# Performance work log

Hardware: AMD Instinct MI355X
Metric: run time of the kernel (lower is better)

## Reference

```python
import jax, jax.numpy as jnp
import numpy as np

N = 2048
IN_C, HID, LAT = 128, 128, 64
E_SPARSE = 65536


def gcn_conv(x, W, b, src, dst, w, n):
    # PyG GCNConv: h = D^-1/2 (A+I) D^-1/2 (x W) + b  (self-loops already in edge list)
    deg = jax.ops.segment_sum(w, dst, num_segments=n)
    dinv = jnp.where(deg > 0, jax.lax.rsqrt(deg), 0.0)
    norm = dinv[src] * w * dinv[dst]            # [E]
    h = x @ W                                   # [N, out]
    agg = jax.ops.segment_sum(h[src] * norm[:, None], dst, num_segments=n)
    return agg + b


def setup_inputs() -> dict:
    key = jax.random.key(0)
    ks = jax.random.split(key, 9)
    x = jax.random.normal(ks[0], (N, IN_C), jnp.float32)
    masked_y = jax.random.normal(ks[1], (N, N), jnp.float32)
    edge_index = jax.random.randint(ks[2], (2, E_SPARSE), 0, N, dtype=jnp.int32)
    s = 0.05
    W1 = jax.random.normal(ks[3], (IN_C, HID), jnp.float32) * s
    b1 = jnp.zeros((HID,), jnp.float32)
    Wmu = jax.random.normal(ks[4], (HID, LAT), jnp.float32) * s
    bmu = jnp.zeros((LAT,), jnp.float32)
    Wls = jax.random.normal(ks[5], (HID, LAT), jnp.float32) * s
    bls = jnp.zeros((LAT,), jnp.float32)
    return {"x": x, "masked_y": masked_y, "W1": W1, "b1": b1,
            "Wmu": Wmu, "bmu": bmu, "Wls": Wls, "bls": bls,
            "edge_index": edge_index}


def reference(x, masked_y, W1, b1, Wmu, bmu, Wls, bls, edge_index):
    n = x.shape[0]
    half = n // 2
    # masking leaves only the top-left [half, half] block of masked_y nonzero;
    # dense_to_sparse on that block -> all half*half (row, col) pairs (entries != 0 a.s.)
    rows = jnp.repeat(jnp.arange(half, dtype=edge_index.dtype), half)
    cols = jnp.tile(jnp.arange(half, dtype=edge_index.dtype), half)
    y_w = jax.nn.sigmoid(masked_y[:half, :half].reshape(-1))
    loop = jnp.arange(n, dtype=edge_index.dtype)
    src = jnp.concatenate([edge_index[0], rows, loop])
    dst = jnp.concatenate([edge_index[1], cols, loop])
    w = jnp.concatenate([jnp.ones((edge_index.shape[1],), x.dtype), y_w,
                         jnp.ones((n,), x.dtype)])
    hidden = jax.nn.relu(gcn_conv(x, W1, b1, src, dst, w, n))
    z_mu = gcn_conv(hidden, Wmu, bmu, src, dst, w, n)
    z_logstd = gcn_conv(hidden, Wls, bls, src, dst, w, n)
    return (z_mu, z_logstd)
```

## Files before the change

### kernel.cpp

```cpp
#include <hip/hip_runtime.h>

#define NN 2048
#define HALF 1024
#define CC 128
#define EE 65536
#define CAP 128

typedef unsigned short u16;

__device__ __forceinline__ float sigm(float v){ return 1.0f/(1.0f + __expf(-v)); }

__device__ __forceinline__ float dinv_lo(int i, const int* __restrict__ cnt,
                                         const float* __restrict__ colsum){
  return rsqrtf(1.0f + (float)cnt[i] + colsum[i]);
}
__device__ __forceinline__ float dinv_any(int i, const int* __restrict__ cnt,
                                          const float* __restrict__ colsum){
  float cs = (i < HALF) ? colsum[i] : 0.0f;
  return rsqrtf(1.0f + (float)cnt[i] + cs);
}

__global__ __launch_bounds__(256) void k_prep(
    const float* __restrict__ my, const int* __restrict__ ei,
    const float* __restrict__ bmu, const float* __restrict__ bls,
    float* __restrict__ SpRaw, float* __restrict__ colsum,
    int* __restrict__ cnt, u16* __restrict__ bucket,
    float* __restrict__ out)
{
  int b = blockIdx.x, t = threadIdx.x;
  if (b < 128) {
    int c0 = t*4;
    float cs0=0.f, cs1=0.f, cs2=0.f, cs3=0.f;
    #pragma unroll 2
    for (int rr=0; rr<8; ++rr){
      int r = b*8 + rr;
      float4 v = *(const float4*)(my + (size_t)r*NN + c0);
      float s0=sigm(v.x), s1=sigm(v.y), s2=sigm(v.z), s3=sigm(v.w);
      *(float4*)(SpRaw + (size_t)r*HALF + c0) = make_float4(s0,s1,s2,s3);
      cs0+=s0; cs1+=s1; cs2+=s2; cs3+=s3;
    }
    atomicAdd(&colsum[c0+0], cs0);
    atomicAdd(&colsum[c0+1], cs1);
    atomicAdd(&colsum[c0+2], cs2);
    atomicAdd(&colsum[c0+3], cs3);
  } else {
    int bb = b - 128;
    int gid = bb*256 + t;
    int g4 = (gid & 15)*4;
    const float* bbias = (gid < 32768) ? bmu : bls;
    ((float4*)out)[gid] = make_float4(bbias[g4], bbias[g4+1], bbias[g4+2], bbias[g4+3]);
    int e = bb*256 + t;
    int s = ei[e], d = ei[EE + e];
    int slot = atomicAdd(&cnt[d], 1);
    if (slot < CAP) bucket[d*CAP + slot] = (u16)s;
  }
}

__global__ __launch_bounds__(256) void k_agg1(
  const float* __restrict__ SpRaw, const float* __restrict__ x,
  const int* __restrict__ cnt, const float* __restrict__ colsum,
  const u16* __restrict__ bucket,
  float* __restrict__ SP, float* __restrict__ DP)
{
  int b = blockIdx.x, t = threadIdx.x;
  if (b < 512) {
    __shared__ float srow[128];
    int chunk = b & 7, r0 = chunk*128;
    if (t < 128) srow[t] = dinv_lo(r0 + t, cnt, colsum);
    __syncthreads();
    int lane = t & 63, f0 = lane*2;
    int dbase = (b>>3)*16 + (t>>6)*4;
    float a00=0.f,a01=0.f,a10=0.f,a11=0.f,a20=0.f,a21=0.f,a30=0.f,a31=0.f;
    #pragma unroll 2
    for (int rr=0; rr<128; rr+=4){
      int r = r0 + rr;
      float2 v0 = *(const float2*)(x + (size_t)(r+0)*CC + f0);
      float2 v1 = *(const float2*)(x + (size_t)(r+1)*CC + f0);
      float2 v2 = *(const float2*)(x + (size_t)(r+2)*CC + f0);
      float2 v3 = *(const float2*)(x + (size_t)(r+3)*CC + f0);
      float4 s0 = *(const float4*)(SpRaw + (size_t)(r+0)*HALF + dbase);
      float4 s1 = *(const float4*)(SpRaw + (size_t)(r+1)*HALF + dbase);
      float4 s2 = *(const float4*)(SpRaw + (size_t)(r+2)*HALF + dbase);
      float4 s3 = *(const float4*)(SpRaw + (size_t)(r+3)*HALF + dbase);
      float c0 = srow[rr+0], c1 = srow[rr+1], c2 = srow[rr+2], c3 = srow[rr+3];
      float fx, fy;
      fx = v0.x*c0; fy = v0.y*c0;
      a00=fmaf(s0.x,fx,a00); a01=fmaf(s0.x,fy,a01);
      a10=fmaf(s0.y,fx,a10); a11=fmaf(s0.y,fy,a11);
      a20=fmaf(s0.z,fx,a20); a21=fmaf(s0.z,fy,a21);
      a30=fmaf(s0.w,fx,a30); a31=fmaf(s0.w,fy,a31);
      fx = v1.x*c1; fy = v1.y*c1;
      a00=fmaf(s1.x,fx,a00); a01=fmaf(s1.x,fy,a01);
      a10=fmaf(s1.y,fx,a10); a11=fmaf(s1.y,fy,a11);
      a20=fmaf(s1.z,fx,a20); a21=fmaf(s1.z,fy,a21);
      a30=fmaf(s1.w,fx,a30); a31=fmaf(s1.w,fy,a31);
      fx = v2.x*c2; fy = v2.y*c2;
      a00=fmaf(s2.x,fx,a00); a01=fmaf(s2.x,fy,a01);
      a10=fmaf(s2.y,fx,a10); a11=fmaf(s2.y,fy,a11);
      a20=fmaf(s2.z,fx,a20); a21=fmaf(s2.z,fy,a21);
      a30=fmaf(s2.w,fx,a30); a31=fmaf(s2.w,fy,a31);
      fx = v3.x*c3; fy = v3.y*c3;
      a00=fmaf(s3.x,fx,a00); a01=fmaf(s3.x,fy,a01);
      a10=fmaf(s3.y,fx,a10); a11=fmaf(s3.y,fy,a11);
      a20=fmaf(s3.z,fx,a20); a21=fmaf(s3.z,fy,a21);
      a30=fmaf(s3.w,fx,a30); a31=fmaf(s3.w,fy,a31);
    }
    float d0=dinv_lo(dbase+0,cnt,colsum), d1=dinv_lo(dbase+1,cnt,colsum);
    float d2=dinv_lo(dbase+2,cnt,colsum), d3=dinv_lo(dbase+3,cnt,colsum);
    float* o = DP + ((size_t)chunk*HALF + dbase)*CC + f0;
    o[0*CC+0]=a00*d0; o[0*CC+1]=a01*d0;
    o[1*CC+0]=a10*d1; o[1*CC+1]=a11*d1;
    o[2*CC+0]=a20*d2; o[2*CC+1]=a21*d2;
    o[3*CC+0]=a30*d3; o[3*CC+1]=a31*d3;
  } else {
    __shared__ float sdinv[NN];
    #pragma unroll
    for (int i=0;i<8;i++){
      int j = i*256 + t;
      float cs = (j < HALF) ? colsum[j] : 0.0f;
      sdinv[j] = rsqrtf(1.0f + (float)cnt[j] + cs);
    }
    __syncthreads();
    int w = t>>6, hw = (t>>5)&1, l = t&31;
    int d = (b-512)*8 + w*2 + hw;
    int f0 = l*4;
    float dd = sdinv[d];
    float4 sv = *(const float4*)(x + (size_t)d*CC + f0);
    float ax=dd*sv.x, ay=dd*sv.y, az=dd*sv.z, aw=dd*sv.w;
    int m = cnt[d]; m = m > CAP ? CAP : m;
    const u16* bk = bucket + d*CAP;
    int j = 0;
    for (; j+1 < m; j += 2){
      unsigned pr = *(const unsigned*)(bk + j);
      int s0 = pr & 0xffff, s1 = pr >> 16;
      float w0 = sdinv[s0], w1 = sdinv[s1];
      float4 v0 = *(const float4*)(x + (size_t)s0*CC + f0);
      float4 v1 = *(const float4*)(x + (size_t)s1*CC + f0);
      ax=fmaf(w0,v0.x,ax); ay=fmaf(w0,v0.y,ay); az=fmaf(w0,v0.z,az); aw=fmaf(w0,v0.w,aw);
      ax=fmaf(w1,v1.x,ax); ay=fmaf(w1,v1.y,ay); az=fmaf(w1,v1.z,az); aw=fmaf(w1,v1.w,aw);
    }
    if (j < m){
      int s0 = bk[j];
      float w0 = sdinv[s0];
      float4 v0 = *(const float4*)(x + (size_t)s0*CC + f0);
      ax=fmaf(w0,v0.x,ax); ay=fmaf(w0,v0.y,ay); az=fmaf(w0,v0.z,az); aw=fmaf(w0,v0.w,aw);
    }
    *(float4*)(SP + (size_t)d*CC + f0) = make_float4(dd*ax, dd*ay, dd*az, dd*aw);
  }
}

__global__ __launch_bounds__(256) void k_mid(
  const float* __restrict__ SP, const float* __restrict__ DP,
  const float* __restrict__ b1, const float* __restrict__ W1,
  const float* __restrict__ Wmu, const float* __restrict__ Wls,
  const int* __restrict__ cnt, const float* __restrict__ colsum,
  float* __restrict__ Gm)
{
  __shared__ float la[4][CC];
  __shared__ float lb[4][CC];
  int b = blockIdx.x, t = threadIdx.x;
  int row0 = b*4;
  #pragma unroll
  for (int i=0;i<2;i++){
    int idx = i*256 + t;
    int r = row0 + (idx>>7), c = idx & 127;
    float v = SP[(size_t)r*CC + c];
    if (r < HALF){
      #pragma unroll
      for (int k=0;k<8;k++) v += DP[((size_t)k*HALF + r)*CC + c];
    }
    la[idx>>7][c] = v;
  }
  __syncthreads();
  int f = t & 127, rh = t >> 7;
  {
    const float4* a0 = (const float4*)la[rh*2+0];
    const float4* a1 = (const float4*)la[rh*2+1];
    float o0=0.f, o1=0.f;
    #pragma unroll 4
    for (int k4=0;k4<32;k4++){
      float4 v0=a0[k4], v1=a1[k4];
      float w0 = W1[(k4*4+0)*CC + f];
      float w1 = W1[(k4*4+1)*CC + f];
      float w2 = W1[(k4*4+2)*CC + f];
      float w3 = W1[(k4*4+3)*CC + f];
      o0=fmaf(v0.x,w0,o0); o0=fmaf(v0.y,w1,o0); o0=fmaf(v0.z,w2,o0); o0=fmaf(v0.w,w3,o0);
      o1=fmaf(v1.x,w0,o1); o1=fmaf(v1.y,w1,o1); o1=fmaf(v1.z,w2,o1); o1=fmaf(v1.w,w3,o1);
    }
    float bb = b1[f];
    o0 += bb; o1 += bb;
    lb[rh*2+0][f] = o0 > 0.f ? o0 : 0.f;
    lb[rh*2+1][f] = o1 > 0.f ? o1 : 0.f;
  }
  __syncthreads();
  {
    int g = f & 63;
    const float* W = (f < 64) ? Wmu : Wls;
    const float4* a0 = (const float4*)lb[rh*2+0];
    const float4* a1 = (const float4*)lb[rh*2+1];
    float o0=0.f, o1=0.f;
    #pragma unroll 4
    for (int k4=0;k4<32;k4++){
      float4 v0=a0[k4], v1=a1[k4];
      float w0 = W[(k4*4+0)*64 + g];
      float w1 = W[(k4*4+1)*64 + g];
      float w2 = W[(k4*4+2)*64 + g];
      float w3 = W[(k4*4+3)*64 + g];
      o0=fmaf(v0.x,w0,o0); o0=fmaf(v0.y,w1,o0); o0=fmaf(v0.z,w2,o0); o0=fmaf(v0.w,w3,o0);
      o1=fmaf(v1.x,w0,o1); o1=fmaf(v1.y,w1,o1); o1=fmaf(v1.z,w2,o1); o1=fmaf(v1.w,w3,o1);
    }
    int rA = row0 + rh*2;
    Gm[(size_t)(rA+0)*CC + f] = o0 * dinv_any(rA+0, cnt, colsum);
    Gm[(size_t)(rA+1)*CC + f] = o1 * dinv_any(rA+1, cnt, colsum);
  }
}

__global__ __launch_bounds__(256) void k_agg2(
  const float* __restrict__ SpRaw, const float* __restrict__ Gm,
  const int* __restrict__ cnt, const float* __restrict__ colsum,
  const u16* __restrict__ bucket, float* __restrict__ out)
{
  int b = blockIdx.x, t = threadIdx.x;
  if (b < 512) {
    int lane = t & 63, f0 = lane*2;
    size_t obase = (f0 < 64) ? 0 : (size_t)NN*64;
    int g0 = f0 & 63;
    int dbase = (b>>3)*16 + (t>>6)*4;
    int r0 = (b&7)*128;
    float a00=0.f,a01=0.f,a10=0.f,a11=0.f,a20=0.f,a21=0.f,a30=0.f,a31=0.f;
    #pragma unroll 2
    for (int rr=0; rr<128; rr+=4){
      int r = r0 + rr;
      float2 v0 = *(const float2*)(Gm + (size_t)(r+0)*CC + f0);
      float2 v1 = *(const float2*)(Gm + (size_t)(r+1)*CC + f0);
      float2 v2 = *(const float2*)(Gm + (size_t)(r+2)*CC + f0);
      float2 v3 = *(const float2*)(Gm + (size_t)(r+3)*CC + f0);
      float4 s0 = *(const float4*)(SpRaw + (size_t)(r+0)*HALF + dbase);
      float4 s1 = *(const float4*)(SpRaw + (size_t)(r+1)*HALF + dbase);
      float4 s2 = *(const float4*)(SpRaw + (size_t)(r+2)*HALF + dbase);
      float4 s3 = *(const float4*)(SpRaw + (size_t)(r+3)*HALF + dbase);
      a00=fmaf(s0.x,v0.x,a00); a01=fmaf(s0.x,v0.y,a01);
      a10=fmaf(s0.y,v0.x,a10); a11=fmaf(s0.y,v0.y,a11);
      a20=fmaf(s0.z,v0.x,a20); a21=fmaf(s0.z,v0.y,a21);
      a30=fmaf(s0.w,v0.x,a30); a31=fmaf(s0.w,v0.y,a31);
      a00=fmaf(s1.x,v1.x,a00); a01=fmaf(s1.x,v1.y,a01);
      a10=fmaf(s1.y,v1.x,a10); a11=fmaf(s1.y,v1.y,a11);
      a20=fmaf(s1.z,v1.x,a20); a21=fmaf(s1.z,v1.y,a21);
      a30=fmaf(s1.w,v1.x,a30); a31=fmaf(s1.w,v1.y,a31);
      a00=fmaf(s2.x,v2.x,a00); a01=fmaf(s2.x,v2.y,a01);
      a10=fmaf(s2.y,v2.x,a10); a11=fmaf(s2.y,v2.y,a11);
      a20=fmaf(s2.z,v2.x,a20); a21=fmaf(s2.z,v2.y,a21);
      a30=fmaf(s2.w,v2.x,a30); a31=fmaf(s2.w,v2.y,a31);
      a00=fmaf(s3.x,v3.x,a00); a01=fmaf(s3.x,v3.y,a01);
      a10=fmaf(s3.y,v3.x,a10); a11=fmaf(s3.y,v3.y,a11);
      a20=fmaf(s3.z,v3.x,a20); a21=fmaf(s3.z,v3.y,a21);
      a30=fmaf(s3.w,v3.x,a30); a31=fmaf(s3.w,v3.y,a31);
    }
    float d0=dinv_lo(dbase+0,cnt,colsum), d1=dinv_lo(dbase+1,cnt,colsum);
    float d2=dinv_lo(dbase+2,cnt,colsum), d3=dinv_lo(dbase+3,cnt,colsum);
    float* o = out + obase + (size_t)dbase*64 + g0;
    atomicAdd(o + 0*64 + 0, a00*d0); atomicAdd(o + 0*64 + 1, a01*d0);
    atomicAdd(o + 1*64 + 0, a10*d1); atomicAdd(o + 1*64 + 1, a11*d1);
    atomicAdd(o + 2*64 + 0, a20*d2); atomicAdd(o + 2*64 + 1, a21*d2);
    atomicAdd(o + 3*64 + 0, a30*d3); atomicAdd(o + 3*64 + 1, a31*d3);
  } else {
    int w = t>>6, hw = (t>>5)&1, l = t&31;
    int d = (b-512)*8 + w*2 + hw;
    int f0 = l*4;
    size_t obase = (f0 < 64) ? 0 : (size_t)NN*64;
    int g0 = f0 & 63;
    float4 a = *(const float4*)(Gm + (size_t)d*CC + f0);
    float ax=a.x, ay=a.y, az=a.z, aw=a.w;
    int m = cnt[d]; m = m > CAP ? CAP : m;
    const u16* bk = bucket + d*CAP;
    int j = 0;
    for (; j+1 < m; j += 2){
      unsigned pr = *(const unsigned*)(bk + j);
      int s0 = pr & 0xffff, s1 = pr >> 16;
      float4 v0 = *(const float4*)(Gm + (size_t)s0*CC + f0);
      float4 v1 = *(const float4*)(Gm + (size_t)s1*CC + f0);
      ax += v0.x + v1.x; ay += v0.y + v1.y;
      az += v0.z + v1.z; aw += v0.w + v1.w;
    }
    if (j < m){
      int s0 = bk[j];
      float4 v0 = *(const float4*)(Gm + (size_t)s0*CC + f0);
      ax += v0.x; ay += v0.y; az += v0.z; aw += v0.w;
    }
    float dd = dinv_any(d, cnt, colsum);
    float* o = out + obase + (size_t)d*64 + g0;
    atomicAdd(o + 0, dd*ax); atomicAdd(o + 1, dd*ay);
    atomicAdd(o + 2, dd*az); atomicAdd(o + 3, dd*aw);
  }
}

extern "C" void kernel_launch(void* const* d_in, const int* in_sizes, int n_in,
                              void* d_out, int out_size, void* d_ws, size_t ws_size,
                              hipStream_t stream)
{
  (void)in_sizes; (void)n_in; (void)out_size; (void)ws_size;
  const float* x   = (const float*)d_in[0];
  const float* my  = (const float*)d_in[1];
  const float* W1  = (const float*)d_in[2];
  const float* b1  = (const float*)d_in[3];
  const float* Wmu = (const float*)d_in[4];
  const float* bmu = (const float*)d_in[5];
  const float* Wls = (const float*)d_in[6];
  const float* bls = (const float*)d_in[7];
  const int*   ei  = (const int*)d_in[8];
  float* out = (float*)d_out;
  char* ws = (char*)d_ws;

  int*   cnt    = (int*)  (ws + 0);
  float* colsum = (float*)(ws + 8192);
  u16*   bucket = (u16*)  (ws + 12288);
  float* SpRaw  = (float*)(ws + 536576);
  float* Gm     = (float*)(ws + 4730880);
  float* SP     = (float*)(ws + 5779456);
  float* DP     = (float*)(ws + 6828032);

  hipMemsetAsync(ws, 0, 12288, stream);
  k_prep<<<384, 256, 0, stream>>>(my, ei, bmu, bls, SpRaw, colsum, cnt, bucket, out);
  k_agg1<<<768, 256, 0, stream>>>(SpRaw, x, cnt, colsum, bucket, SP, DP);
  k_mid <<<512, 256, 0, stream>>>(SP, DP, b1, W1, Wmu, Wls, cnt, colsum, Gm);
  k_agg2<<<768, 256, 0, stream>>>(SpRaw, Gm, cnt, colsum, bucket, out);
}
```

Before: 160.4 us.

## Apply W1 before first aggregation by computing x@W1 in prep kernel

Reorders the first GCN layer from aggregate-then-project to project-then-aggregate, matching the reference order. x@W1 is computed into a new H0 buffer inside k_prep, using 256 extra blocks that run alongside the sigmoid and bucket work, and k_agg1 now aggregates H0. This drops the W1 matmul and one sync from k_mid, which now only adds bias, applies relu and does the mu/logstd projection. The matmul moves off the critical middle kernel into the prep stage, at the cost of an extra 1 MB intermediate write and read.

```diff
diff --git a/kernel.cpp b/kernel.cpp
--- a/kernel.cpp
+++ b/kernel.cpp
@@ -21,13 +21,22 @@
 }
 
 __global__ __launch_bounds__(256) void k_prep(
-    const float* __restrict__ my, const int* __restrict__ ei,
+    const float* __restrict__ my, const int* __restrict__ ei, const float* __restrict__ x,
+    const float* __restrict__ W1,
     const float* __restrict__ bmu, const float* __restrict__ bls,
     float* __restrict__ SpRaw, float* __restrict__ colsum,
-    int* __restrict__ cnt, u16* __restrict__ bucket,
+    int* __restrict__ cnt, u16* __restrict__ bucket, float* __restrict__ H0,
     float* __restrict__ out)
 {
+  __shared__ float la[8][CC];
   int b = blockIdx.x, t = threadIdx.x;
+  int gid = b*256 + t;
+  if (gid < 65536) {
+    int g4 = (gid & 15)*4;
+    const float* bb = (gid < 32768) ? bmu : bls;
+    ((float4*)out)[gid] = make_float4(bb[g4], bb[g4+1], bb[g4+2], bb[g4+3]);
+  }
+
   if (b < 128) {
     int c0 = t*4;
     float cs0=0.f, cs1=0.f, cs2=0.f, cs3=0.f;
@@ -43,21 +52,50 @@
     atomicAdd(&colsum[c0+1], cs1);
     atomicAdd(&colsum[c0+2], cs2);
     atomicAdd(&colsum[c0+3], cs3);
+  } else if (b < 256) {
+    int e0 = (b-128)*512 + t;
+    #pragma unroll
+    for (int i=0;i<2;i++){
+      int e = e0 + i*256;
+      int s = ei[e], d = ei[EE + e];
+      int slot = atomicAdd(&cnt[d], 1);
+      if (slot < CAP) bucket[d*CAP + slot] = (u16)s;
+    }
   } else {
-    int bb = b - 128;
-    int gid = bb*256 + t;
-    int g4 = (gid & 15)*4;
-    const float* bbias = (gid < 32768) ? bmu : bls;
-    ((float4*)out)[gid] = make_float4(bbias[g4], bbias[g4+1], bbias[g4+2], bbias[g4+3]);
-    int e = bb*256 + t;
-    int s = ei[e], d = ei[EE + e];
-    int slot = atomicAdd(&cnt[d], 1);
-    if (slot < CAP) bucket[d*CAP + slot] = (u16)s;
+    int row0 = (b-256)*8;
+    #pragma unroll
+    for (int i=0;i<4;i++){
+      int idx = i*256 + t;
+      la[idx>>7][idx&127] = x[(size_t)row0*CC + idx];
+    }
+    __syncthreads();
+    int f = t & 127, rh = t >> 7;
+    const float4* a0 = (const float4*)la[rh*4+0];
+    const float4* a1 = (const float4*)la[rh*4+1];
+    const float4* a2 = (const float4*)la[rh*4+2];
+    const float4* a3 = (const float4*)la[rh*4+3];
+    float o0=0.f, o1=0.f, o2=0.f, o3=0.f;
+    #pragma unroll 4
+    for (int k4=0;k4<32;k4++){
+      float4 v0=a0[k4], v1=a1[k4], v2=a2[k4], v3=a3[k4];
+      float w0 = W1[(k4*4+0)*CC + f];
+      float w1 = W1[(k4*4+1)*CC + f];
+      float w2 = W1[(k4*4+2)*CC + f];
+      float w3 = W1[(k4*4+3)*CC + f];
+      o0=fmaf(v0.x,w0,o0); o0=fmaf(v0.y,w1,o0); o0=fmaf(v0.z,w2,o0); o0=fmaf(v0.w,w3,o0);
+      o1=fmaf(v1.x,w0,o1); o1=fmaf(v1.y,w1,o1); o1=fmaf(v1.z,w2,o1); o1=fmaf(v1.w,w3,o1);
+      o2=fmaf(v2.x,w0,o2); o2=fmaf(v2.y,w1,o2); o2=fmaf(v2.z,w2,o2); o2=fmaf(v2.w,w3,o2);
+      o3=fmaf(v3.x,w0,o3); o3=fmaf(v3.y,w1,o3); o3=fmaf(v3.z,w2,o3); o3=fmaf(v3.w,w3,o3);
+    }
+    H0[(size_t)(row0 + rh*4 + 0)*CC + f] = o0;
+    H0[(size_t)(row0 + rh*4 + 1)*CC + f] = o1;
+    H0[(size_t)(row0 + rh*4 + 2)*CC + f] = o2;
+    H0[(size_t)(row0 + rh*4 + 3)*CC + f] = o3;
   }
 }
 
 __global__ __launch_bounds__(256) void k_agg1(
-  const float* __restrict__ SpRaw, const float* __restrict__ x,
+  const float* __restrict__ SpRaw, const float* __restrict__ H0,
   const int* __restrict__ cnt, const float* __restrict__ colsum,
   const u16* __restrict__ bucket,
   float* __restrict__ SP, float* __restrict__ DP)
@@ -74,10 +112,10 @@
     #pragma unroll 2
     for (int rr=0; rr<128; rr+=4){
       int r = r0 + rr;
-      float2 v0 = *(const float2*)(x + (size_t)(r+0)*CC + f0);
-      float2 v1 = *(const float2*)(x + (size_t)(r+1)*CC + f0);
-      float2 v2 = *(const float2*)(x + (size_t)(r+2)*CC + f0);
-      float2 v3 = *(const float2*)(x + (size_t)(r+3)*CC + f0);
+      float2 v0 = *(const float2*)(H0 + (size_t)(r+0)*CC + f0);
+      float2 v1 = *(const float2*)(H0 + (size_t)(r+1)*CC + f0);
+      float2 v2 = *(const float2*)(H0 + (size_t)(r+2)*CC + f0);
+      float2 v3 = *(const float2*)(H0 + (size_t)(r+3)*CC + f0);
       float4 s0 = *(const float4*)(SpRaw + (size_t)(r+0)*HALF + dbase);
       float4 s1 = *(const float4*)(SpRaw + (size_t)(r+1)*HALF + dbase);
       float4 s2 = *(const float4*)(SpRaw + (size_t)(r+2)*HALF + dbase);
@@ -125,7 +163,7 @@
     int d = (b-512)*8 + w*2 + hw;
     int f0 = l*4;
     float dd = sdinv[d];
-    float4 sv = *(const float4*)(x + (size_t)d*CC + f0);
+    float4 sv = *(const float4*)(H0 + (size_t)d*CC + f0);
     float ax=dd*sv.x, ay=dd*sv.y, az=dd*sv.z, aw=dd*sv.w;
     int m = cnt[d]; m = m > CAP ? CAP : m;
     const u16* bk = bucket + d*CAP;
@@ -134,15 +172,15 @@
       unsigned pr = *(const unsigned*)(bk + j);
       int s0 = pr & 0xffff, s1 = pr >> 16;
       float w0 = sdinv[s0], w1 = sdinv[s1];
-      float4 v0 = *(const float4*)(x + (size_t)s0*CC + f0);
-      float4 v1 = *(const float4*)(x + (size_t)s1*CC + f0);
+      float4 v0 = *(const float4*)(H0 + (size_t)s0*CC + f0);
+      float4 v1 = *(const float4*)(H0 + (size_t)s1*CC + f0);
       ax=fmaf(w0,v0.x,ax); ay=fmaf(w0,v0.y,ay); az=fmaf(w0,v0.z,az); aw=fmaf(w0,v0.w,aw);
       ax=fmaf(w1,v1.x,ax); ay=fmaf(w1,v1.y,ay); az=fmaf(w1,v1.z,az); aw=fmaf(w1,v1.w,aw);
     }
     if (j < m){
       int s0 = bk[j];
       float w0 = sdinv[s0];
-      float4 v0 = *(const float4*)(x + (size_t)s0*CC + f0);
+      float4 v0 = *(const float4*)(H0 + (size_t)s0*CC + f0);
       ax=fmaf(w0,v0.x,ax); ay=fmaf(w0,v0.y,ay); az=fmaf(w0,v0.z,az); aw=fmaf(w0,v0.w,aw);
     }
     *(float4*)(SP + (size_t)d*CC + f0) = make_float4(dd*ax, dd*ay, dd*az, dd*aw);
@@ -151,13 +189,12 @@
 
 __global__ __launch_bounds__(256) void k_mid(
   const float* __restrict__ SP, const float* __restrict__ DP,
-  const float* __restrict__ b1, const float* __restrict__ W1,
+  const float* __restrict__ b1,
   const float* __restrict__ Wmu, const float* __restrict__ Wls,
   const int* __restrict__ cnt, const float* __restrict__ colsum,
   float* __restrict__ Gm)
 {
   __shared__ float la[4][CC];
-  __shared__ float lb[4][CC];
   int b = blockIdx.x, t = threadIdx.x;
   int row0 = b*4;
   #pragma unroll
@@ -169,50 +206,28 @@
       #pragma unroll
       for (int k=0;k<8;k++) v += DP[((size_t)k*HALF + r)*CC + c];
     }
-    la[idx>>7][c] = v;
+    v += b1[c];
+    la[idx>>7][c] = v > 0.f ? v : 0.f;
   }
   __syncthreads();
-  int f = t & 127, rh = t >> 7;
-  {
-    const float4* a0 = (const float4*)la[rh*2+0];
-    const float4* a1 = (const float4*)la[rh*2+1];
-    float o0=0.f, o1=0.f;
-    #pragma unroll 4
-    for (int k4=0;k4<32;k4++){
-      float4 v0=a0[k4], v1=a1[k4];
-      float w0 = W1[(k4*4+0)*CC + f];
-      float w1 = W1[(k4*4+1)*CC + f];
-      float w2 = W1[(k4*4+2)*CC + f];
-      float w3 = W1[(k4*4+3)*CC + f];
-      o0=fmaf(v0.x,w0,o0); o0=fmaf(v0.y,w1,o0); o0=fmaf(v0.z,w2,o0); o0=fmaf(v0.w,w3,o0);
-      o1=fmaf(v1.x,w0,o1); o1=fmaf(v1.y,w1,o1); o1=fmaf(v1.z,w2,o1); o1=fmaf(v1.w,w3,o1);
-    }
-    float bb = b1[f];
-    o0 += bb; o1 += bb;
-    lb[rh*2+0][f] = o0 > 0.f ? o0 : 0.f;
-    lb[rh*2+1][f] = o1 > 0.f ? o1 : 0.f;
-  }
-  __syncthreads();
-  {
-    int g = f & 63;
-    const float* W = (f < 64) ? Wmu : Wls;
-    const float4* a0 = (const float4*)lb[rh*2+0];
-    const float4* a1 = (const float4*)lb[rh*2+1];
-    float o0=0.f, o1=0.f;
-    #pragma unroll 4
-    for (int k4=0;k4<32;k4++){
-      float4 v0=a0[k4], v1=a1[k4];
-      float w0 = W[(k4*4+0)*64 + g];
-      float w1 = W[(k4*4+1)*64 + g];
-      float w2 = W[(k4*4+2)*64 + g];
-      float w3 = W[(k4*4+3)*64 + g];
-      o0=fmaf(v0.x,w0,o0); o0=fmaf(v0.y,w1,o0); o0=fmaf(v0.z,w2,o0); o0=fmaf(v0.w,w3,o0);
-      o1=fmaf(v1.x,w0,o1); o1=fmaf(v1.y,w1,o1); o1=fmaf(v1.z,w2,o1); o1=fmaf(v1.w,w3,o1);
-    }
-    int rA = row0 + rh*2;
-    Gm[(size_t)(rA+0)*CC + f] = o0 * dinv_any(rA+0, cnt, colsum);
-    Gm[(size_t)(rA+1)*CC + f] = o1 * dinv_any(rA+1, cnt, colsum);
-  }
+  int f = t & 127, rh = t >> 7, g = f & 63;
+  const float* W = (f < 64) ? Wmu : Wls;
+  const float4* a0 = (const float4*)la[rh*2+0];
+  const float4* a1 = (const float4*)la[rh*2+1];
+  float o0=0.f, o1=0.f;
+  #pragma unroll 4
+  for (int k4=0;k4<32;k4++){
+    float4 v0=a0[k4], v1=a1[k4];
+    float w0 = W[(k4*4+0)*64 + g];
+    float w1 = W[(k4*4+1)*64 + g];
+    float w2 = W[(k4*4+2)*64 + g];
+    float w3 = W[(k4*4+3)*64 + g];
+    o0=fmaf(v0.x,w0,o0); o0=fmaf(v0.y,w1,o0); o0=fmaf(v0.z,w2,o0); o0=fmaf(v0.w,w3,o0);
+    o1=fmaf(v1.x,w0,o1); o1=fmaf(v1.y,w1,o1); o1=fmaf(v1.z,w2,o1); o1=fmaf(v1.w,w3,o1);
+  }
+  int rA = row0 + rh*2;
+  Gm[(size_t)(rA+0)*CC + f] = o0 * dinv_any(rA+0, cnt, colsum);
+  Gm[(size_t)(rA+1)*CC + f] = o1 * dinv_any(rA+1, cnt, colsum);
 }
 
 __global__ __launch_bounds__(256) void k_agg2(
@@ -315,13 +330,15 @@
   float* colsum = (float*)(ws + 8192);
   u16*   bucket = (u16*)  (ws + 12288);
   float* SpRaw  = (float*)(ws + 536576);
-  float* Gm     = (float*)(ws + 4730880);
-  float* SP     = (float*)(ws + 5779456);
-  float* DP     = (float*)(ws + 6828032);
+  float* H0     = (float*)(ws + 4730880);
+  float* Gm     = (float*)(ws + 5779456);
+  float* SP     = (float*)(ws + 6828032);
+  float* DP     = (float*)(ws + 7876608);
 
   hipMemsetAsync(ws, 0, 12288, stream);
-  k_prep<<<384, 256, 0, stream>>>(my, ei, bmu, bls, SpRaw, colsum, cnt, bucket, out);
-  k_agg1<<<768, 256, 0, stream>>>(SpRaw, x, cnt, colsum, bucket, SP, DP);
-  k_mid <<<512, 256, 0, stream>>>(SP, DP, b1, W1, Wmu, Wls, cnt, colsum, Gm);
+  k_prep<<<512, 256, 0, stream>>>(my, ei, x, W1, bmu, bls,
+                                  SpRaw, colsum, cnt, bucket, H0, out);
+  k_agg1<<<768, 256, 0, stream>>>(SpRaw, H0, cnt, colsum, bucket, SP, DP);
+  k_mid <<<512, 256, 0, stream>>>(SP, DP, b1, Wmu, Wls, cnt, colsum, Gm);
   k_agg2<<<768, 256, 0, stream>>>(SpRaw, Gm, cnt, colsum, bucket, out);
 }
```

New measurement: 156.7 us. 2.3% less time.
